# Optimization experiments

Measured on AMD Instinct MI355X. Metric: run time of the kernel, lower is better.

## Reference

```python
import jax, jax.numpy as jnp
import numpy as np

Q_MAX = 127.0
EPS = 1e-5


def setup_inputs() -> dict:
    key = jax.random.key(0)
    k1, k2, k3, k4 = jax.random.split(key, 4)
    M, K, N = 4096, 4096, 11008
    x = jax.random.normal(k1, (M, K), dtype=jnp.float16)
    # pre-quantized int8 weight (per-channel symmetric) + its float scale per output channel
    weight = jax.random.randint(k2, (N, K), -127, 128, dtype=jnp.int32).astype(jnp.int8)
    scale_channel = (jax.random.uniform(k3, (N,), dtype=jnp.float32) * 0.01 + 1e-4)
    bias = jax.random.normal(k4, (N,), dtype=jnp.float16)
    return {"x": x, "weight": weight, "scale_channel": scale_channel, "bias": bias}


def reference(x, weight, scale_channel, bias):
    # per-token abs-max quantization of activations (quant_act)
    scales = jnp.max(jnp.abs(x), axis=-1, keepdims=True).astype(jnp.float32)  # [M,1]
    scales = jnp.clip(scales, EPS, None) / Q_MAX
    q_x = jnp.round(x.astype(jnp.float32) / scales).astype(jnp.int8)  # [M,K]
    # int8 GEMM with int32 accumulation: [M,K] @ [K,N]
    acc = jax.lax.dot_general(
        q_x, weight.T,
        dimension_numbers=(((1,), (0,)), ((), ())),
        preferred_element_type=jnp.int32,
    )  # [M,N] int32
    # dequantize: per-token act scale * per-channel weight scale, then cast to fp16
    out = (acc.astype(jnp.float32) * scales * scale_channel[None, :]).astype(jnp.float16)
    out = out + bias  # fp16 bias add
    return out
```

## Files before the change

kernel.cpp:

```cpp
#include <hip/hip_runtime.h>
#include <hip/hip_fp16.h>
#include <hip/hip_cooperative_groups.h>
#include <stdint.h>

namespace cg = cooperative_groups;

#define Q_MAX 127.0f
#define EPSQ  1e-5f

typedef int   v4i __attribute__((ext_vector_type(4)));
typedef float v4f __attribute__((ext_vector_type(4)));

__device__ __forceinline__ int pack4i(int a, int b, int c, int d) {
    return (a & 0xff) | ((b & 0xff) << 8) | ((c & 0xff) << 16) | (d << 24);
}
__device__ __forceinline__ float ep(float v, float b) {
    return __half2float(__hadd(__float2half(v), __float2half(b)));
}
__device__ __forceinline__ void async16(const void* g, const void* l) {
    __builtin_amdgcn_global_load_lds((const __attribute__((address_space(1))) uint32_t*)g,
                                     (__attribute__((address_space(3))) uint32_t*)l,
                                     16, 0, 0);
}

#define BMc 128
#define BNc 128
#define BKc 64
#define CTHR 256
#define CGRID 688

__global__ __launch_bounds__(CTHR, 3) void w8a8_coop(const float* __restrict__ x,
                                                     const int* __restrict__ w32,
                                                     const float* __restrict__ scw,
                                                     const float* __restrict__ bias,
                                                     float* __restrict__ out,
                                                     int8_t* __restrict__ w8,
                                                     int8_t* __restrict__ xq,
                                                     float* __restrict__ scales,
                                                     int M, int N, int K) {
    __shared__ __align__(16) int8_t As[BMc * BKc];
    __shared__ __align__(16) int8_t Bs[BNc * BKc];

    const int t   = threadIdx.x;
    const int bid = blockIdx.x;

    {
        const int T   = CGRID * CTHR;
        const int tg  = bid * CTHR + t;
        const v4i* src = (const v4i*)w32;
        int* dst = (int*)w8;
        const int tot = (N * K) >> 2;
#pragma unroll 4
        for (int h = tg; h < tot; h += T) {
            v4i u = __builtin_nontemporal_load(src + h);
            dst[h] = pack4i(u[0], u[1], u[2], u[3]);
        }
    }
    {
        const int row = bid * 8 + (t >> 5);
        const int l2  = t & 31;
        if (bid < 512 && row < M) {
            const v4f* p = (const v4f*)(x + (size_t)row * K);
            float amax = 0.f;
            for (int i = 0; i < K / 128; ++i) {
                v4f v = p[l2 + 32 * i];
                amax = fmaxf(amax, fmaxf(fmaxf(fabsf(v[0]), fabsf(v[1])),
                                         fmaxf(fabsf(v[2]), fabsf(v[3]))));
            }
#pragma unroll
            for (int off = 16; off >= 1; off >>= 1) amax = fmaxf(amax, __shfl_xor(amax, off));
            const float s  = fmaxf(amax, EPSQ) / Q_MAX;
            const float rs = 1.0f / s;
            if (l2 == 0) scales[row] = s;
            int* q4 = (int*)(xq + (size_t)row * K);
            for (int i = 0; i < K / 128; ++i) {
                v4f v = p[l2 + 32 * i];
                q4[l2 + 32 * i] = pack4i(__float2int_rn(v[0] * rs), __float2int_rn(v[1] * rs),
                                         __float2int_rn(v[2] * rs), __float2int_rn(v[3] * rs));
            }
        }
    }
    __threadfence();
    cg::this_grid().sync();

    const int w  = t >> 6;
    const int l  = t & 63;
    const int wm = w & 1;
    const int wn = w >> 1;

    const int rA0 = w * 32 + (l >> 2);
    const int rA1 = rA0 + 16;
    const int cq0 = (l & 3) ^ ((rA0 >> 1) & 3);
    const int cq1 = (l & 3) ^ ((rA1 >> 1) & 3);
    int8_t* lA0 = As + w * 2048;
    int8_t* lA1 = As + w * 2048 + 1024;
    int8_t* lB0 = Bs + w * 2048;
    int8_t* lB1 = Bs + w * 2048 + 1024;

    const int fr   = l & 15;
    const int fc   = (l >> 4) ^ ((fr >> 1) & 3);
    const int aoff = (wm * 64 + fr) * 64 + fc * 16;
    const int boff = (wn * 64 + fr) * 64 + fc * 16;

    const int nbn  = N / BNc;
    const int nblk = (M / BMc) * nbn;

    for (int sidx = bid; sidx < nblk; sidx += CGRID) {
        int L = sidx;
        if ((nblk & 7) == 0) L = (sidx & 7) * (nblk >> 3) + (sidx >> 3);
        const int bm = (L / nbn) * BMc;
        const int bn = (L % nbn) * BNc;

        const int8_t* gA0 = xq + (size_t)(bm + rA0) * K + cq0 * 16;
        const int8_t* gA1 = xq + (size_t)(bm + rA1) * K + cq1 * 16;
        const int8_t* gB0 = w8 + (size_t)(bn + rA0) * K + cq0 * 16;
        const int8_t* gB1 = w8 + (size_t)(bn + rA1) * K + cq1 * 16;

        v4i acc[4][4] = {};

        for (int kt = 0; kt < K; kt += BKc) {
            __syncthreads();
            async16(gA0 + kt, lA0);
            async16(gA1 + kt, lA1);
            async16(gB0 + kt, lB0);
            async16(gB1 + kt, lB1);
            __syncthreads();

            v4i a[4], b[4];
#pragma unroll
            for (int i = 0; i < 4; ++i) a[i] = *(const v4i*)(As + aoff + i * 16 * 64);
#pragma unroll
            for (int j = 0; j < 4; ++j) b[j] = *(const v4i*)(Bs + boff + j * 16 * 64);
#pragma unroll
            for (int i = 0; i < 4; ++i)
#pragma unroll
                for (int j = 0; j < 4; ++j)
                    acc[i][j] = __builtin_amdgcn_mfma_i32_16x16x64_i8(a[i], b[j], acc[i][j], 0, 0, 0);
        }

        const int colb = bn + wn * 64 + fr;
#pragma unroll
        for (int i = 0; i < 4; ++i) {
            const int m0 = bm + wm * 64 + i * 16 + (l >> 4) * 4;
#pragma unroll
            for (int r = 0; r < 4; ++r) {
                const float sm = scales[m0 + r];
                float* orow = out + (size_t)(m0 + r) * N;
#pragma unroll
                for (int j = 0; j < 4; ++j) {
                    const int n = colb + j * 16;
                    __builtin_nontemporal_store(ep((float)acc[i][j][r] * sm * scw[n], bias[n]), orow + n);
                }
            }
        }
    }
}

#define BM 128
#define BN 256
#define BK 64
#define NTHR 512

__global__ __launch_bounds__(NTHR) void w8a8_one(const float* __restrict__ x,
                                                 const int* __restrict__ w32,
                                                 const float* __restrict__ scw,
                                                 const float* __restrict__ bias,
                                                 float* __restrict__ out,
                                                 int M, int N, int K) {
    __shared__ __align__(16) int8_t As[2][BM * BK];
    __shared__ __align__(16) int8_t Bs[2][BN * BK];
    __shared__ float sS[BM];
    __shared__ float sR[BM];

    const int t  = threadIdx.x;
    const int w  = t >> 6;
    const int l  = t & 63;
    const int wm = w & 1;
    const int wn = w >> 1;

    const int nbn  = N / BN;
    const int nblk = (M / BM) * nbn;
    int L = blockIdx.x;
    if ((nblk & 7) == 0) {
        const int c = nblk >> 3;
        L = (L & 7) * c + (L >> 3);
    }
    const int bm = (L / nbn) * BM;
    const int bn = (L % nbn) * BN;

    {
        const int row = t >> 2;
        const int seg = t & 3;
        const float4* p = (const float4*)(x + (size_t)(bm + row) * K) + seg;
        float amax = 0.f;
        for (int j = 0; j < K / 16; ++j) {
            float4 v = p[j * 4];
            amax = fmaxf(amax, fmaxf(fmaxf(fabsf(v.x), fabsf(v.y)),
                                     fmaxf(fabsf(v.z), fabsf(v.w))));
        }
        amax = fmaxf(amax, __shfl_xor(amax, 1));
        amax = fmaxf(amax, __shfl_xor(amax, 2));
        if (seg == 0) {
            const float s = fmaxf(amax, EPSQ) / Q_MAX;
            sS[row] = s;
            sR[row] = 1.0f / s;
        }
    }
    __syncthreads();

    const int ra  = t >> 2;
    const int sa  = t & 3;
    const float rs = sR[ra];
    const float4* gA = (const float4*)(x + (size_t)(bm + ra) * K) + sa * 4;
    const int offA = ra * 64 + ((sa ^ ((ra >> 1) & 3)) << 4);

    const int rb  = t >> 1;
    const int hb  = t & 1;
    const int swb = (rb >> 1) & 3;
    const int* gB = w32 + (size_t)(bn + rb) * K + hb * 32;
    const int offB0 = rb * 64 + ((((hb * 2)    ) ^ swb) << 4);
    const int offB1 = rb * 64 + ((((hb * 2) + 1) ^ swb) << 4);

    const int fr   = l & 15;
    const int fc   = (l >> 4) ^ ((fr >> 1) & 3);
    const int aoff = (wm * 64 + fr) * 64 + fc * 16;
    const int boff = (wn * 64 + fr) * 64 + fc * 16;

    v4i acc[4][4] = {};
    float4 rA[4];
    v4i    rB[8];

    auto load_tile = [&](int kt) {
#pragma unroll
        for (int i = 0; i < 4; ++i) rA[i] = gA[(kt >> 2) + i];
        const v4i* g4 = (const v4i*)(gB + kt);
#pragma unroll
        for (int i = 0; i < 8; ++i) rB[i] = g4[i];
    };
    auto pack_write = [&](int buf) {
        const float* vals = (const float*)rA;
        int q[16];
#pragma unroll
        for (int i = 0; i < 16; ++i) q[i] = __float2int_rn(vals[i] * rs);
        int pk[4];
#pragma unroll
        for (int c2 = 0; c2 < 4; ++c2)
            pk[c2] = pack4i(q[c2 * 4 + 0], q[c2 * 4 + 1], q[c2 * 4 + 2], q[c2 * 4 + 3]);
        *(int4*)(As[buf] + offA) = *(const int4*)pk;
        int p0[4] = { pack4i(rB[0][0],rB[0][1],rB[0][2],rB[0][3]),
                      pack4i(rB[1][0],rB[1][1],rB[1][2],rB[1][3]),
                      pack4i(rB[2][0],rB[2][1],rB[2][2],rB[2][3]),
                      pack4i(rB[3][0],rB[3][1],rB[3][2],rB[3][3]) };
        int p1[4] = { pack4i(rB[4][0],rB[4][1],rB[4][2],rB[4][3]),
                      pack4i(rB[5][0],rB[5][1],rB[5][2],rB[5][3]),
                      pack4i(rB[6][0],rB[6][1],rB[6][2],rB[6][3]),
                      pack4i(rB[7][0],rB[7][1],rB[7][2],rB[7][3]) };
        *(int4*)(Bs[buf] + offB0) = *(const int4*)p0;
        *(int4*)(Bs[buf] + offB1) = *(const int4*)p1;
    };

    load_tile(0);
    pack_write(0);

    int cur = 0;
#pragma unroll 1
    for (int kt = 0; kt < K; kt += BK) {
        __syncthreads();
        const bool more = (kt + BK) < K;
        if (more) load_tile(kt + BK);

        const int8_t* Ab = As[cur];
        const int8_t* Bb = Bs[cur];
        v4i a[4], b[4];
#pragma unroll
        for (int i = 0; i < 4; ++i) a[i] = *(const v4i*)(Ab + aoff + i * 16 * 64);
#pragma unroll
        for (int j = 0; j < 4; ++j) b[j] = *(const v4i*)(Bb + boff + j * 16 * 64);
#pragma unroll
        for (int i = 0; i < 4; ++i)
#pragma unroll
            for (int j = 0; j < 4; ++j)
                acc[i][j] = __builtin_amdgcn_mfma_i32_16x16x64_i8(a[i], b[j], acc[i][j], 0, 0, 0);

        __syncthreads();
        if (more) pack_write(cur ^ 1);
        cur ^= 1;
    }

    const int colb = bn + wn * 64 + fr;
#pragma unroll
    for (int i = 0; i < 4; ++i) {
        const int r0 = wm * 64 + i * 16 + (l >> 4) * 4;
#pragma unroll
        for (int r = 0; r < 4; ++r) {
            const float sm = sS[r0 + r];
            float* orow = out + (size_t)(bm + r0 + r) * N;
#pragma unroll
            for (int j = 0; j < 4; ++j) {
                const int n = colb + j * 16;
                __builtin_nontemporal_store(ep((float)acc[i][j][r] * sm * scw[n], bias[n]), orow + n);
            }
        }
    }
}

extern "C" void kernel_launch(void* const* d_in, const int* in_sizes, int n_in,
                              void* d_out, int out_size, void* d_ws, size_t ws_size,
                              hipStream_t stream) {
    const float* x    = (const float*)d_in[0];
    const int*   wgt  = (const int*)d_in[1];
    const float* scw  = (const float*)d_in[2];
    const float* bias = (const float*)d_in[3];
    float* out = (float*)d_out;

    int N = in_sizes[2];
    int K = in_sizes[1] / N;
    int M = in_sizes[0] / K;

    const size_t need = (size_t)N * K + (size_t)M * K + (size_t)M * 4;
    bool done = false;
    if (ws_size >= need && (M % BMc) == 0 && (N % BNc) == 0 && (K % 128) == 0) {
        int8_t* w8     = (int8_t*)d_ws;
        int8_t* xq     = w8 + (size_t)N * K;
        float*  scales = (float*)(xq + (size_t)M * K);
        void* args[] = { (void*)&x, (void*)&wgt, (void*)&scw, (void*)&bias, (void*)&out,
                         (void*)&w8, (void*)&xq, (void*)&scales,
                         (void*)&M, (void*)&N, (void*)&K };
        hipError_t err = hipLaunchCooperativeKernel((const void*)w8a8_coop,
                                                    dim3(CGRID), dim3(CTHR),
                                                    args, 0, stream);
        done = (err == hipSuccess);
    }
    if (!done) {
        const int nblk = (M / BM) * (N / BN);
        w8a8_one<<<dim3(nblk), NTHR, 0, stream>>>(x, wgt, scw, bias, out, M, N, K);
    }
}
```

Measured before the change: 753.0 us.

## Double-buffer LDS tiles in coop GEMM and raise grid occupancy

```diff
diff --git a/kernel.cpp b/kernel.cpp
--- a/kernel.cpp
+++ b/kernel.cpp
@@ -22,14 +22,19 @@
                                      (__attribute__((address_space(3))) uint32_t*)l,
                                      16, 0, 0);
 }
+__device__ __forceinline__ void pipe_barrier() {
+    asm volatile("s_waitcnt vmcnt(0)" ::: "memory");
+    __builtin_amdgcn_s_barrier();
+    asm volatile("" ::: "memory");
+}
 
 #define BMc 128
 #define BNc 128
 #define BKc 64
 #define CTHR 256
-#define CGRID 688
-
-__global__ __launch_bounds__(CTHR, 3) void w8a8_coop(const float* __restrict__ x,
+#define CGRID 1024
+
+__global__ __launch_bounds__(CTHR, 4) void w8a8_coop(const float* __restrict__ x,
                                                      const int* __restrict__ w32,
                                                      const float* __restrict__ scw,
                                                      const float* __restrict__ bias,
@@ -38,11 +43,13 @@
                                                      int8_t* __restrict__ xq,
                                                      float* __restrict__ scales,
                                                      int M, int N, int K) {
-    __shared__ __align__(16) int8_t As[BMc * BKc];
-    __shared__ __align__(16) int8_t Bs[BNc * BKc];
+    __shared__ __align__(16) int8_t As[2][BMc * BKc];
+    __shared__ __align__(16) int8_t Bs[2][BNc * BKc];
 
     const int t   = threadIdx.x;
     const int bid = blockIdx.x;
+    const int w   = t >> 6;
+    const int l   = t & 63;
 
     {
         const int T   = CGRID * CTHR;
@@ -57,34 +64,32 @@
         }
     }
     {
-        const int row = bid * 8 + (t >> 5);
-        const int l2  = t & 31;
-        if (bid < 512 && row < M) {
+        const int row = bid * 4 + w;
+        if (row < M) {
             const v4f* p = (const v4f*)(x + (size_t)row * K);
+            const int npl = K / 256;
             float amax = 0.f;
-            for (int i = 0; i < K / 128; ++i) {
-                v4f v = p[l2 + 32 * i];
+            for (int i = 0; i < npl; ++i) {
+                v4f v = p[l + 64 * i];
                 amax = fmaxf(amax, fmaxf(fmaxf(fabsf(v[0]), fabsf(v[1])),
                                          fmaxf(fabsf(v[2]), fabsf(v[3]))));
             }
 #pragma unroll
-            for (int off = 16; off >= 1; off >>= 1) amax = fmaxf(amax, __shfl_xor(amax, off));
+            for (int off = 32; off >= 1; off >>= 1) amax = fmaxf(amax, __shfl_xor(amax, off));
             const float s  = fmaxf(amax, EPSQ) / Q_MAX;
-            const float rs = 1.0f / s;
-            if (l2 == 0) scales[row] = s;
+            const float rsc = 1.0f / s;
+            if (l == 0) scales[row] = s;
             int* q4 = (int*)(xq + (size_t)row * K);
-            for (int i = 0; i < K / 128; ++i) {
-                v4f v = p[l2 + 32 * i];
-                q4[l2 + 32 * i] = pack4i(__float2int_rn(v[0] * rs), __float2int_rn(v[1] * rs),
-                                         __float2int_rn(v[2] * rs), __float2int_rn(v[3] * rs));
+            for (int i = 0; i < npl; ++i) {
+                v4f v = p[l + 64 * i];
+                q4[l + 64 * i] = pack4i(__float2int_rn(v[0] * rsc), __float2int_rn(v[1] * rsc),
+                                        __float2int_rn(v[2] * rsc), __float2int_rn(v[3] * rsc));
             }
         }
     }
     __threadfence();
     cg::this_grid().sync();
 
-    const int w  = t >> 6;
-    const int l  = t & 63;
     const int wm = w & 1;
     const int wn = w >> 1;
 
@@ -92,50 +97,59 @@
     const int rA1 = rA0 + 16;
     const int cq0 = (l & 3) ^ ((rA0 >> 1) & 3);
     const int cq1 = (l & 3) ^ ((rA1 >> 1) & 3);
-    int8_t* lA0 = As + w * 2048;
-    int8_t* lA1 = As + w * 2048 + 1024;
-    int8_t* lB0 = Bs + w * 2048;
-    int8_t* lB1 = Bs + w * 2048 + 1024;
 
     const int fr   = l & 15;
     const int fc   = (l >> 4) ^ ((fr >> 1) & 3);
     const int aoff = (wm * 64 + fr) * 64 + fc * 16;
     const int boff = (wn * 64 + fr) * 64 + fc * 16;
 
+    const int nbm  = M / BMc;
     const int nbn  = N / BNc;
-    const int nblk = (M / BMc) * nbn;
-
-    for (int sidx = bid; sidx < nblk; sidx += CGRID) {
+    const int nblk = nbm * nbn;
+
+    for (int sidx = bid; sidx < nblk; sidx += gridDim.x) {
         int L = sidx;
         if ((nblk & 7) == 0) L = (sidx & 7) * (nblk >> 3) + (sidx >> 3);
-        const int bm = (L / nbn) * BMc;
-        const int bn = (L % nbn) * BNc;
+        const int bm = (L % nbm) * BMc;
+        const int bn = (L / nbm) * BNc;
 
         const int8_t* gA0 = xq + (size_t)(bm + rA0) * K + cq0 * 16;
         const int8_t* gA1 = xq + (size_t)(bm + rA1) * K + cq1 * 16;
         const int8_t* gB0 = w8 + (size_t)(bn + rA0) * K + cq0 * 16;
         const int8_t* gB1 = w8 + (size_t)(bn + rA1) * K + cq1 * 16;
 
+        auto stage = [&](int buf, int kt) {
+            async16(gA0 + kt, As[buf] + w * 2048);
+            async16(gA1 + kt, As[buf] + w * 2048 + 1024);
+            async16(gB0 + kt, Bs[buf] + w * 2048);
+            async16(gB1 + kt, Bs[buf] + w * 2048 + 1024);
+        };
+
         v4i acc[4][4] = {};
 
+        stage(0, 0);
+        pipe_barrier();
+
+        int cur = 0;
+#pragma unroll 1
         for (int kt = 0; kt < K; kt += BKc) {
-            __syncthreads();
-            async16(gA0 + kt, lA0);
-            async16(gA1 + kt, lA1);
-            async16(gB0 + kt, lB0);
-            async16(gB1 + kt, lB1);
-            __syncthreads();
+            if (kt + BKc < K) stage(cur ^ 1, kt + BKc);
 
             v4i a[4], b[4];
 #pragma unroll
-            for (int i = 0; i < 4; ++i) a[i] = *(const v4i*)(As + aoff + i * 16 * 64);
-#pragma unroll
-            for (int j = 0; j < 4; ++j) b[j] = *(const v4i*)(Bs + boff + j * 16 * 64);
+            for (int i = 0; i < 4; ++i) a[i] = *(const v4i*)(As[cur] + aoff + i * 16 * 64);
+#pragma unroll
+            for (int j = 0; j < 4; ++j) b[j] = *(const v4i*)(Bs[cur] + boff + j * 16 * 64);
+            __builtin_amdgcn_s_setprio(1);
 #pragma unroll
             for (int i = 0; i < 4; ++i)
 #pragma unroll
                 for (int j = 0; j < 4; ++j)
                     acc[i][j] = __builtin_amdgcn_mfma_i32_16x16x64_i8(a[i], b[j], acc[i][j], 0, 0, 0);
+            __builtin_amdgcn_s_setprio(0);
+
+            pipe_barrier();
+            cur ^= 1;
         }
 
         const int colb = bn + wn * 64 + fr;
@@ -319,7 +333,8 @@
 
     const size_t need = (size_t)N * K + (size_t)M * K + (size_t)M * 4;
     bool done = false;
-    if (ws_size >= need && (M % BMc) == 0 && (N % BNc) == 0 && (K % 128) == 0) {
+    if (ws_size >= need && (M % BMc) == 0 && (N % BNc) == 0 && (K % 256) == 0 &&
+        M <= CGRID * 4) {
         int8_t* w8     = (int8_t*)d_ws;
         int8_t* xq     = w8 + (size_t)N * K;
         float*  scales = (float*)(xq + (size_t)M * K);
```

Measured after the change: 756.2 us. Within noise of the previous version (+0.4%).
